# Kernel optimization log

Hardware: AMD Instinct MI355X
Metric: run time of the kernel (lower is better)

Reference implementation:

```python
import jax, jax.numpy as jnp
import numpy as np

EPS = 1e-5


def setup_inputs() -> dict:
    key = jax.random.key(0)
    ks = jax.random.split(key, 8)
    N, M, D = 8192, 8192, 512
    s = 1.0 / np.sqrt(D)
    return {
        "x": jax.random.normal(ks[0], (N, D), jnp.float32),
        "x_hat": jax.random.normal(ks[1], (1, M, D), jnp.float32),
        "Wq": jax.random.normal(ks[2], (D, D), jnp.float32) * s,
        "bq": jnp.zeros((D,), jnp.float32),
        "Wk": jax.random.normal(ks[3], (D, D), jnp.float32) * s,
        "bk": jnp.zeros((D,), jnp.float32),
        "Wv": jax.random.normal(ks[4], (D, D), jnp.float32) * s,
        "bv": jnp.zeros((D,), jnp.float32),
        "Wout": jax.random.normal(ks[5], (D, 2 * D), jnp.float32) * s,
        "bout": jnp.zeros((D,), jnp.float32),
        "gamma": jnp.ones((D,), jnp.float32),
        "beta": jnp.zeros((D,), jnp.float32),
    }


def reference(x, x_hat, Wq, bq, Wk, bk, Wv, bv, Wout, bout, gamma, beta):
    D = x.shape[-1]
    # LayerNorm over last dim
    mu = jnp.mean(x, axis=-1, keepdims=True)
    var = jnp.mean(jnp.square(x - mu), axis=-1, keepdims=True)
    xn = (x - mu) * jax.lax.rsqrt(var + EPS) * gamma + beta
    xr = xn.reshape(1, -1, D)                                   # [1, N, D]
    q = jnp.einsum('bnd,ed->bne', xr, Wq) + bq                  # [1, N, E]
    k = jnp.einsum('bmd,ed->bme', x_hat, Wk) + bk               # [1, M, E]
    qk = jnp.einsum('bne,bme->bnm', q, k) / jnp.sqrt(jnp.float32(D))
    score = jax.nn.softmax(qk, axis=-1)                         # [1, N, M]
    attn = jnp.einsum('bnm,bme->bne', score, k)                 # K used as values
    out_v = jnp.einsum('bne,fe->bnf', attn, Wv) + bv            # v-proj AFTER attention
    cat = jnp.concatenate([q, out_v], axis=-1)                  # [1, N, 2E]
    out = jnp.einsum('bnc,dc->bnd', cat, Wout) + bout           # [1, N, D]
    return out + xr
```

## Files before the change

kernel.cpp:

```cpp
#include <hip/hip_runtime.h>

typedef __attribute__((ext_vector_type(8))) short short8;
typedef __attribute__((ext_vector_type(4))) short short4v;
typedef __attribute__((ext_vector_type(4))) float f32x4;
typedef __attribute__((ext_vector_type(2))) float f32x2;

#define MFMA(a,b,c) __builtin_amdgcn_mfma_f32_16x16x32_bf16((a),(b),(c),0,0,0)

__device__ __forceinline__ short f2b(float f) {
  unsigned u = __builtin_bit_cast(unsigned, f);
  unsigned r = (u + 0x7fffu + ((u >> 16) & 1u)) >> 16;
  return (short)r;
}
__device__ __forceinline__ float b2f(short h) {
  unsigned u = ((unsigned)(unsigned short)h) << 16;
  return __builtin_bit_cast(float, u);
}
__device__ __forceinline__ unsigned pack2(float a, float b) {
  return (unsigned)(unsigned short)f2b(a) | ((unsigned)(unsigned short)f2b(b) << 16);
}

__device__ __forceinline__ float wred(float v) {
  #pragma unroll
  for (int m = 32; m; m >>= 1) v += __shfl_xor(v, m, 64);
  return v;
}

__device__ __forceinline__ void glds16(const short* g, short* l) {
  __builtin_amdgcn_global_load_lds(
      (const __attribute__((address_space(1))) unsigned*)g,
      (__attribute__((address_space(3))) unsigned*)l, 16, 0, 0);
}

__global__ __launch_bounds__(256) void cvt_kernel(const float* __restrict__ src,
                                                  short* __restrict__ dst, int n4) {
  int i = blockIdx.x * 256 + threadIdx.x;
  if (i < n4) {
    f32x4 v = *(const f32x4*)(src + (size_t)i * 4);
    short4v o = { f2b(v[0]), f2b(v[1]), f2b(v[2]), f2b(v[3]) };
    *(short4v*)(dst + (size_t)i * 4) = o;
  }
}

__global__ __launch_bounds__(256) void w2_kernel(const float* __restrict__ Wout,
                                                 const float* __restrict__ Wv,
                                                 const float* __restrict__ bvv,
                                                 const float* __restrict__ bout,
                                                 short* __restrict__ W12,
                                                 float* __restrict__ biasf) {
  int d0 = blockIdx.x * 4, tid = threadIdx.x;
  float a[4][2] = {};
  float ab[4] = {};
  for (int f = 0; f < 512; ++f) {
    f32x2 vv = *(const f32x2*)(Wv + (size_t)f * 512 + 2 * tid);
    float bvf = bvv[f];
    #pragma unroll
    for (int dd = 0; dd < 4; ++dd) {
      float wdf = Wout[(size_t)(d0 + dd) * 1024 + 512 + f];
      a[dd][0] = fmaf(wdf, vv[0], a[dd][0]);
      a[dd][1] = fmaf(wdf, vv[1], a[dd][1]);
      ab[dd] = fmaf(wdf, bvf, ab[dd]);
    }
  }
  #pragma unroll
  for (int dd = 0; dd < 4; ++dd)
    *(unsigned*)&W12[(size_t)(d0 + dd) * 1024 + 512 + 2 * tid] = pack2(a[dd][0], a[dd][1]);
  if (tid == 0) {
    #pragma unroll
    for (int dd = 0; dd < 4; ++dd) biasf[d0 + dd] = bout[d0 + dd] + ab[dd];
  }
}

__global__ __launch_bounds__(256) void ln_kernel(const float* __restrict__ x,
                                                 const float* __restrict__ gamma,
                                                 const float* __restrict__ beta,
                                                 float* __restrict__ xnf,
                                                 short* __restrict__ xnb) {
  int n = blockIdx.x, tid = threadIdx.x;
  int wid = tid >> 6, lane = tid & 63;
  f32x2 v = *(const f32x2*)(x + (size_t)n * 512 + tid * 2);
  __shared__ float red[8];
  float ws = wred(v[0] + v[1]);
  if (!lane) red[wid] = ws;
  __syncthreads();
  float mu = (red[0] + red[1] + red[2] + red[3]) * (1.f / 512.f);
  float d0 = v[0] - mu, d1 = v[1] - mu;
  ws = wred(d0 * d0 + d1 * d1);
  if (!lane) red[4 + wid] = ws;
  __syncthreads();
  float var = (red[4] + red[5] + red[6] + red[7]) * (1.f / 512.f);
  float rs = rsqrtf(var + 1e-5f);
  int c = tid * 2;
  float o0 = d0 * rs * gamma[c] + beta[c];
  float o1 = d1 * rs * gamma[c + 1] + beta[c + 1];
  *(f32x2*)(xnf + (size_t)n * 512 + c) = f32x2{ o0, o1 };
  *(unsigned*)(xnb + (size_t)n * 512 + c) = pack2(o0, o1);
}

template<int MODE>
__global__ __launch_bounds__(256, 2) void gemm_nt(
    const short* __restrict__ A, const short* __restrict__ B,
    int K, int lda, int ldb,
    const float* __restrict__ bias,
    short* __restrict__ Cb, int ldc, int coff,
    short* __restrict__ CT, int ldct,
    const float* __restrict__ resid, float* __restrict__ Cf) {
  __shared__ short As[128][72];
  __shared__ short Bs[128][72];
  int tid = threadIdx.x;
  int w = tid >> 6, lane = tid & 63;
  int li = lane & 15, g = lane >> 4;
  int wr = w >> 1, wc = w & 1;
  int bm = blockIdx.x, bn = blockIdx.y;
  f32x4 acc[4][4] = {};
  int nK = K >> 6;
  for (int kk = 0; kk < nK; ++kk) {
    short8 av[4], bv4[4];
    #pragma unroll
    for (int c = 0; c < 4; ++c) {
      int q = c * 256 + tid;
      int r = q >> 3, s = q & 7;
      av[c]  = *(const short8*)(A + (size_t)(bm * 128 + r) * lda + kk * 64 + s * 8);
      bv4[c] = *(const short8*)(B + (size_t)(bn * 128 + r) * ldb + kk * 64 + s * 8);
    }
    __syncthreads();
    #pragma unroll
    for (int c = 0; c < 4; ++c) {
      int q = c * 256 + tid;
      int r = q >> 3, s = q & 7;
      *(short8*)&As[r][s * 8] = av[c];
      *(short8*)&Bs[r][s * 8] = bv4[c];
    }
    __syncthreads();
    #pragma unroll
    for (int kc = 0; kc < 2; ++kc) {
      short8 af[4], bfr[4];
      #pragma unroll
      for (int i = 0; i < 4; ++i)
        af[i] = *(const short8*)&As[wr * 64 + i * 16 + li][kc * 32 + (g << 3)];
      #pragma unroll
      for (int j = 0; j < 4; ++j)
        bfr[j] = *(const short8*)&Bs[wc * 64 + j * 16 + li][kc * 32 + (g << 3)];
      #pragma unroll
      for (int i = 0; i < 4; ++i)
        #pragma unroll
        for (int j = 0; j < 4; ++j)
          acc[i][j] = MFMA(af[i], bfr[j], acc[i][j]);
    }
  }
  int row0 = bm * 128 + wr * 64, col0 = bn * 128 + wc * 64;
  #pragma unroll
  for (int i = 0; i < 4; ++i) {
    #pragma unroll
    for (int j = 0; j < 4; ++j) {
      int col = col0 + j * 16 + li;
      float bcol = bias[col];
      #pragma unroll
      for (int r = 0; r < 4; ++r) {
        int row = row0 + i * 16 + (g << 2) + r;
        float vv = acc[i][j][r] + bcol;
        if (MODE == 2) {
          Cf[(size_t)row * 512 + col] = vv + resid[(size_t)row * 512 + col];
        } else {
          Cb[(size_t)row * ldc + coff + col] = f2b(vv);
        }
      }
    }
  }
  if (MODE == 1) {
    #pragma unroll
    for (int i2 = 0; i2 < 2; ++i2) {
      int base = row0 + i2 * 32;
      #pragma unroll
      for (int j = 0; j < 4; ++j) {
        int col = col0 + j * 16 + li;
        float bcol = bias[col];
        #pragma unroll
        for (int r = 0; r < 4; ++r) {
          int s = (g << 2) + r;
          unsigned pk = pack2(acc[i2 * 2][j][r] + bcol, acc[i2 * 2 + 1][j][r] + bcol);
          *(unsigned*)&CT[(size_t)col * ldct + base + 2 * s] = pk;
        }
      }
    }
  }
}

#define SCALE 0.044194173824159216f
__global__ __launch_bounds__(512, 2) void attn_kernel(
    const short* __restrict__ Qg,
    const short* __restrict__ Kg,
    const short* __restrict__ KTg,
    short* __restrict__ U,
    float* __restrict__ lp) {
  __shared__ short Kl[2][32][520];
  __shared__ short Pl[2][128][32];
  int tid = threadIdx.x, w = tid >> 6, lane = tid & 63;
  int li = lane & 15, g = lane >> 4;
  int qb = blockIdx.x >> 2, ms = blockIdx.x & 3;
  int key_base = ms * 2048;

  short8 qf[16];
  {
    size_t row = (size_t)qb * 128 + w * 16 + li;
    const short* qp = Qg + row * 1024 + (g << 3);
    #pragma unroll
    for (int c = 0; c < 16; ++c) qf[c] = *(const short8*)(qp + c * 32);
  }
  f32x4 acc[8][4] = {};
  float lac[4] = {0.f, 0.f, 0.f, 0.f};

  #pragma unroll
  for (int c = 0; c < 4; ++c) {
    int r = c * 8 + w;
    glds16(Kg + (size_t)(key_base + r) * 512 + lane * 8, &Kl[0][r][0]);
  }
  __syncthreads();

  for (int t = 0; t < 64; ++t) {
    int cur = t & 1, nxt = cur ^ 1;
    if (t < 63) {
      #pragma unroll
      for (int c = 0; c < 4; ++c) {
        int r = c * 8 + w;
        glds16(Kg + (size_t)(key_base + (t + 1) * 32 + r) * 512 + lane * 8, &Kl[nxt][r][0]);
      }
    }
    short8 b2[4];
    #pragma unroll
    for (int et = 0; et < 4; ++et) {
      int e = (w << 6) + (et << 4) + li;
      b2[et] = *(const short8*)(KTg + (size_t)e * 8192 + key_base + t * 32 + (g << 3));
    }
    f32x4 s0 = {0, 0, 0, 0}, s1 = {0, 0, 0, 0};
    #pragma unroll
    for (int c = 0; c < 16; ++c) {
      short8 k0 = *(const short8*)&Kl[cur][li][c * 32 + (g << 3)];
      short8 k1 = *(const short8*)&Kl[cur][16 + li][c * 32 + (g << 3)];
      s0 = MFMA(qf[c], k0, s0);
      s1 = MFMA(qf[c], k1, s1);
    }
    #pragma unroll
    for (int r = 0; r < 4; ++r) {
      float p0 = __expf(s0[r] * SCALE);
      float p1 = __expf(s1[r] * SCALE);
      lac[r] += p0 + p1;
      int prow = (w << 4) + (g << 2) + r;
      *(unsigned*)&Pl[cur][prow][2 * li] = pack2(p0, p1);
    }
    __syncthreads();
    #pragma unroll
    for (int qt = 0; qt < 8; ++qt) {
      short8 a = *(const short8*)&Pl[cur][qt * 16 + li][g << 3];
      #pragma unroll
      for (int et = 0; et < 4; ++et)
        acc[qt][et] = MFMA(a, b2[et], acc[qt][et]);
    }
  }

  short* Up = U + (((size_t)ms * 8192) + (size_t)qb * 128) * 512;
  #pragma unroll
  for (int qt = 0; qt < 8; ++qt)
    #pragma unroll
    for (int et = 0; et < 4; ++et)
      #pragma unroll
      for (int r = 0; r < 4; ++r) {
        int row = (qt << 4) + (g << 2) + r;
        int col = (w << 6) + (et << 4) + li;
        Up[(size_t)row * 512 + col] = f2b(acc[qt][et][r]);
      }
  #pragma unroll
  for (int r = 0; r < 4; ++r) {
    float v = lac[r];
    v += __shfl_xor(v, 1, 16);
    v += __shfl_xor(v, 2, 16);
    v += __shfl_xor(v, 4, 16);
    v += __shfl_xor(v, 8, 16);
    if (!li) lp[ms * 8192 + qb * 128 + (w << 4) + (g << 2) + r] = v;
  }
}

__global__ __launch_bounds__(256) void combine_kernel(const short* __restrict__ U,
                                                      const float* __restrict__ lp,
                                                      short* __restrict__ cat2) {
  int idx = blockIdx.x * 256 + threadIdx.x;
  int n = idx >> 6, e8 = (idx & 63) << 3;
  float s[8] = {0, 0, 0, 0, 0, 0, 0, 0};
  float li = 0.f;
  #pragma unroll
  for (int msv = 0; msv < 4; ++msv) {
    short8 v = *(const short8*)(U + ((size_t)msv * 8192 + n) * 512 + e8);
    #pragma unroll
    for (int j = 0; j < 8; ++j) s[j] += b2f(v[j]);
    li += lp[msv * 8192 + n];
  }
  float inv = 1.f / li;
  short8 o;
  #pragma unroll
  for (int j = 0; j < 8; ++j) o[j] = f2b(s[j] * inv);
  *(short8*)(cat2 + (size_t)n * 1024 + 512 + e8) = o;
}

extern "C" void kernel_launch(void* const* d_in, const int* in_sizes, int n_in,
                              void* d_out, int out_size, void* d_ws, size_t ws_size,
                              hipStream_t stream) {
  const float* x     = (const float*)d_in[0];
  const float* xhat  = (const float*)d_in[1];
  const float* Wq    = (const float*)d_in[2];
  const float* bq    = (const float*)d_in[3];
  const float* Wk    = (const float*)d_in[4];
  const float* bk    = (const float*)d_in[5];
  const float* Wv    = (const float*)d_in[6];
  const float* bv    = (const float*)d_in[7];
  const float* Wout  = (const float*)d_in[8];
  const float* bout  = (const float*)d_in[9];
  const float* gamma = (const float*)d_in[10];
  const float* beta  = (const float*)d_in[11];
  float* out = (float*)d_out;

  char* ws = (char*)d_ws;
  const size_t MB = 1024 * 1024;
  float* xnf  = (float*)(ws + 0);
  short* cat2 = (short*)(ws + 16 * MB);
  short* kb   = (short*)(ws + 32 * MB);
  short* ktb  = (short*)(ws + 40 * MB);
  short* W12  = (short*)(ws + 48 * MB);
  float* bsf  = (float*)(ws + 49 * MB);
  float* lp   = (float*)(ws + 49 * MB + 65536);
  short* U    = (short*)(ws + 52 * MB);
  short* xnb  = (short*)(ws + 52 * MB);
  short* xhb  = (short*)(ws + 60 * MB);
  short* Wqb  = (short*)(ws + 68 * MB);
  short* Wkb  = (short*)(ws + 69 * MB);
  (void)ws_size; (void)in_sizes; (void)n_in; (void)out_size;

  cvt_kernel<<<4096, 256, 0, stream>>>(xhat, xhb, 1048576);
  cvt_kernel<<<256, 256, 0, stream>>>(Wq, Wqb, 65536);
  cvt_kernel<<<256, 256, 0, stream>>>(Wk, Wkb, 65536);
  cvt_kernel<<<512, 256, 0, stream>>>(Wout, W12, 131072);
  w2_kernel<<<128, 256, 0, stream>>>(Wout, Wv, bv, bout, W12, bsf);
  ln_kernel<<<8192, 256, 0, stream>>>(x, gamma, beta, xnf, xnb);
  gemm_nt<0><<<dim3(64, 4), 256, 0, stream>>>(xnb, Wqb, 512, 512, 512, bq,
                                              cat2, 1024, 0, nullptr, 0, nullptr, nullptr);
  gemm_nt<1><<<dim3(64, 4), 256, 0, stream>>>(xhb, Wkb, 512, 512, 512, bk,
                                              kb, 512, 0, ktb, 8192, nullptr, nullptr);
  attn_kernel<<<256, 512, 0, stream>>>(cat2, kb, ktb, U, lp);
  combine_kernel<<<2048, 256, 0, stream>>>(U, lp, cat2);
  gemm_nt<2><<<dim3(64, 4), 256, 0, stream>>>(cat2, W12, 1024, 1024, 1024, bsf,
                                              nullptr, 0, 0, nullptr, 0, xnf, out);
}
```

Baseline: 347.9 us.

## Replace scalar Wout·Wv fold with MFMA GEMM, vectorize LayerNorm, add setprio

The scalar w2_kernel that folded Wv into Wout is replaced by three steps: a transposed bf16 conversion of Wv, a small bias-reduction kernel, and the existing MFMA gemm_nt run on bf16 copies. LayerNorm now handles one row per wavefront with 8-wide vector loads and no shared-memory barriers. The K-transpose store in the K-projection GEMM writes 8-byte packed stores, and the attention kernel raises wave priority around its MFMA loops. The weight product is now computed from bf16 inputs instead of fp32, which slightly changes numerics, and the change adds several extra kernel launches.

```diff
diff --git a/kernel.cpp b/kernel.cpp
--- a/kernel.cpp
+++ b/kernel.cpp
@@ -4,6 +4,7 @@
 typedef __attribute__((ext_vector_type(4))) short short4v;
 typedef __attribute__((ext_vector_type(4))) float f32x4;
 typedef __attribute__((ext_vector_type(2))) float f32x2;
+typedef __attribute__((ext_vector_type(2))) unsigned uint2v;
 
 #define MFMA(a,b,c) __builtin_amdgcn_mfma_f32_16x16x32_bf16((a),(b),(c),0,0,0)
 
@@ -42,33 +43,35 @@
   }
 }
 
-__global__ __launch_bounds__(256) void w2_kernel(const float* __restrict__ Wout,
-                                                 const float* __restrict__ Wv,
-                                                 const float* __restrict__ bvv,
-                                                 const float* __restrict__ bout,
-                                                 short* __restrict__ W12,
-                                                 float* __restrict__ biasf) {
-  int d0 = blockIdx.x * 4, tid = threadIdx.x;
-  float a[4][2] = {};
-  float ab[4] = {};
-  for (int f = 0; f < 512; ++f) {
-    f32x2 vv = *(const f32x2*)(Wv + (size_t)f * 512 + 2 * tid);
-    float bvf = bvv[f];
-    #pragma unroll
-    for (int dd = 0; dd < 4; ++dd) {
-      float wdf = Wout[(size_t)(d0 + dd) * 1024 + 512 + f];
-      a[dd][0] = fmaf(wdf, vv[0], a[dd][0]);
-      a[dd][1] = fmaf(wdf, vv[1], a[dd][1]);
-      ab[dd] = fmaf(wdf, bvf, ab[dd]);
-    }
-  }
-  #pragma unroll
-  for (int dd = 0; dd < 4; ++dd)
-    *(unsigned*)&W12[(size_t)(d0 + dd) * 1024 + 512 + 2 * tid] = pack2(a[dd][0], a[dd][1]);
-  if (tid == 0) {
-    #pragma unroll
-    for (int dd = 0; dd < 4; ++dd) biasf[d0 + dd] = bout[d0 + dd] + ab[dd];
-  }
+__global__ __launch_bounds__(256) void tcvt_kernel(const float* __restrict__ src,
+                                                   short* __restrict__ dst) {
+  __shared__ float tile[32][33];
+  int bx = blockIdx.x & 15, by = blockIdx.x >> 4;
+  int tx = threadIdx.x & 31, ty = threadIdx.x >> 5;
+  #pragma unroll
+  for (int i = 0; i < 4; ++i)
+    tile[ty + 8 * i][tx] = src[(size_t)(by * 32 + ty + 8 * i) * 512 + bx * 32 + tx];
+  __syncthreads();
+  #pragma unroll
+  for (int i = 0; i < 4; ++i)
+    dst[(size_t)(bx * 32 + ty + 8 * i) * 512 + by * 32 + tx] = f2b(tile[tx][ty + 8 * i]);
+}
+
+__global__ __launch_bounds__(256) void bsf_kernel(const float* __restrict__ Wout,
+                                                  const float* __restrict__ bvv,
+                                                  const float* __restrict__ bout,
+                                                  float* __restrict__ biasf,
+                                                  float* __restrict__ zb) {
+  int d = blockIdx.x, tid = threadIdx.x;
+  int wid = tid >> 6, lane = tid & 63;
+  __shared__ float red[4];
+  float s = Wout[(size_t)d * 1024 + 512 + tid] * bvv[tid]
+          + Wout[(size_t)d * 1024 + 768 + tid] * bvv[tid + 256];
+  s = wred(s);
+  if (!lane) red[wid] = s;
+  __syncthreads();
+  if (!tid) biasf[d] = bout[d] + red[0] + red[1] + red[2] + red[3];
+  if (d == 0) { zb[tid] = 0.f; zb[tid + 256] = 0.f; }
 }
 
 __global__ __launch_bounds__(256) void ln_kernel(const float* __restrict__ x,
@@ -76,25 +79,29 @@
                                                  const float* __restrict__ beta,
                                                  float* __restrict__ xnf,
                                                  short* __restrict__ xnb) {
-  int n = blockIdx.x, tid = threadIdx.x;
-  int wid = tid >> 6, lane = tid & 63;
-  f32x2 v = *(const f32x2*)(x + (size_t)n * 512 + tid * 2);
-  __shared__ float red[8];
-  float ws = wred(v[0] + v[1]);
-  if (!lane) red[wid] = ws;
-  __syncthreads();
-  float mu = (red[0] + red[1] + red[2] + red[3]) * (1.f / 512.f);
-  float d0 = v[0] - mu, d1 = v[1] - mu;
-  ws = wred(d0 * d0 + d1 * d1);
-  if (!lane) red[4 + wid] = ws;
-  __syncthreads();
-  float var = (red[4] + red[5] + red[6] + red[7]) * (1.f / 512.f);
+  int wid = threadIdx.x >> 6, lane = threadIdx.x & 63;
+  int n = blockIdx.x * 4 + wid;
+  const float* xp = x + (size_t)n * 512 + lane * 8;
+  f32x4 v0 = *(const f32x4*)xp;
+  f32x4 v1 = *(const f32x4*)(xp + 4);
+  float s = v0[0] + v0[1] + v0[2] + v0[3] + v1[0] + v1[1] + v1[2] + v1[3];
+  float mu = wred(s) * (1.f / 512.f);
+  f32x4 d0 = v0 - mu, d1 = v1 - mu;
+  float q = d0[0]*d0[0] + d0[1]*d0[1] + d0[2]*d0[2] + d0[3]*d0[3]
+          + d1[0]*d1[0] + d1[1]*d1[1] + d1[2]*d1[2] + d1[3]*d1[3];
+  float var = wred(q) * (1.f / 512.f);
   float rs = rsqrtf(var + 1e-5f);
-  int c = tid * 2;
-  float o0 = d0 * rs * gamma[c] + beta[c];
-  float o1 = d1 * rs * gamma[c + 1] + beta[c + 1];
-  *(f32x2*)(xnf + (size_t)n * 512 + c) = f32x2{ o0, o1 };
-  *(unsigned*)(xnb + (size_t)n * 512 + c) = pack2(o0, o1);
+  int c = lane * 8;
+  f32x4 g0 = *(const f32x4*)(gamma + c), g1 = *(const f32x4*)(gamma + c + 4);
+  f32x4 b0 = *(const f32x4*)(beta + c),  b1 = *(const f32x4*)(beta + c + 4);
+  f32x4 o0 = d0 * rs * g0 + b0;
+  f32x4 o1 = d1 * rs * g1 + b1;
+  float* op = xnf + (size_t)n * 512 + c;
+  *(f32x4*)op = o0;
+  *(f32x4*)(op + 4) = o1;
+  short8 ob = { f2b(o0[0]), f2b(o0[1]), f2b(o0[2]), f2b(o0[3]),
+                f2b(o1[0]), f2b(o1[1]), f2b(o1[2]), f2b(o1[3]) };
+  *(short8*)(xnb + (size_t)n * 512 + c) = ob;
 }
 
 template<int MODE>
@@ -176,10 +183,12 @@
         int col = col0 + j * 16 + li;
         float bcol = bias[col];
         #pragma unroll
-        for (int r = 0; r < 4; ++r) {
-          int s = (g << 2) + r;
-          unsigned pk = pack2(acc[i2 * 2][j][r] + bcol, acc[i2 * 2 + 1][j][r] + bcol);
-          *(unsigned*)&CT[(size_t)col * ldct + base + 2 * s] = pk;
+        for (int rp = 0; rp < 2; ++rp) {
+          int r = rp * 2;
+          uint2v pk;
+          pk[0] = pack2(acc[i2 * 2][j][r]     + bcol, acc[i2 * 2 + 1][j][r]     + bcol);
+          pk[1] = pack2(acc[i2 * 2][j][r + 1] + bcol, acc[i2 * 2 + 1][j][r + 1] + bcol);
+          *(uint2v*)&CT[(size_t)col * ldct + base + 8 * g + 2 * r] = pk;
         }
       }
     }
@@ -233,6 +242,7 @@
       b2[et] = *(const short8*)(KTg + (size_t)e * 8192 + key_base + t * 32 + (g << 3));
     }
     f32x4 s0 = {0, 0, 0, 0}, s1 = {0, 0, 0, 0};
+    __builtin_amdgcn_s_setprio(1);
     #pragma unroll
     for (int c = 0; c < 16; ++c) {
       short8 k0 = *(const short8*)&Kl[cur][li][c * 32 + (g << 3)];
@@ -240,6 +250,7 @@
       s0 = MFMA(qf[c], k0, s0);
       s1 = MFMA(qf[c], k1, s1);
     }
+    __builtin_amdgcn_s_setprio(0);
     #pragma unroll
     for (int r = 0; r < 4; ++r) {
       float p0 = __expf(s0[r] * SCALE);
@@ -249,6 +260,7 @@
       *(unsigned*)&Pl[cur][prow][2 * li] = pack2(p0, p1);
     }
     __syncthreads();
+    __builtin_amdgcn_s_setprio(1);
     #pragma unroll
     for (int qt = 0; qt < 8; ++qt) {
       short8 a = *(const short8*)&Pl[cur][qt * 16 + li][g << 3];
@@ -256,6 +268,7 @@
       for (int et = 0; et < 4; ++et)
         acc[qt][et] = MFMA(a, b2[et], acc[qt][et]);
     }
+    __builtin_amdgcn_s_setprio(0);
   }
 
   short* Up = U + (((size_t)ms * 8192) + (size_t)qb * 128) * 512;
@@ -320,26 +333,33 @@
 
   char* ws = (char*)d_ws;
   const size_t MB = 1024 * 1024;
-  float* xnf  = (float*)(ws + 0);
-  short* cat2 = (short*)(ws + 16 * MB);
-  short* kb   = (short*)(ws + 32 * MB);
-  short* ktb  = (short*)(ws + 40 * MB);
-  short* W12  = (short*)(ws + 48 * MB);
-  float* bsf  = (float*)(ws + 49 * MB);
-  float* lp   = (float*)(ws + 49 * MB + 65536);
-  short* U    = (short*)(ws + 52 * MB);
-  short* xnb  = (short*)(ws + 52 * MB);
-  short* xhb  = (short*)(ws + 60 * MB);
-  short* Wqb  = (short*)(ws + 68 * MB);
-  short* Wkb  = (short*)(ws + 69 * MB);
+  float* xnf   = (float*)(ws + 0);
+  short* cat2  = (short*)(ws + 16 * MB);
+  short* kb    = (short*)(ws + 32 * MB);
+  short* ktb   = (short*)(ws + 40 * MB);
+  short* W12   = (short*)(ws + 48 * MB);
+  float* bsf   = (float*)(ws + 49 * MB);
+  float* lp    = (float*)(ws + 49 * MB + 65536);
+  short* Woutb = (short*)(ws + 50 * MB);
+  short* WvTb  = (short*)(ws + 51 * MB);
+  float* zb    = (float*)(ws + 51 * MB + 524288);
+  short* U     = (short*)(ws + 52 * MB);
+  short* xnb   = (short*)(ws + 52 * MB);
+  short* xhb   = (short*)(ws + 60 * MB);
+  short* Wqb   = (short*)(ws + 68 * MB);
+  short* Wkb   = (short*)(ws + 69 * MB);
   (void)ws_size; (void)in_sizes; (void)n_in; (void)out_size;
 
   cvt_kernel<<<4096, 256, 0, stream>>>(xhat, xhb, 1048576);
   cvt_kernel<<<256, 256, 0, stream>>>(Wq, Wqb, 65536);
   cvt_kernel<<<256, 256, 0, stream>>>(Wk, Wkb, 65536);
   cvt_kernel<<<512, 256, 0, stream>>>(Wout, W12, 131072);
-  w2_kernel<<<128, 256, 0, stream>>>(Wout, Wv, bv, bout, W12, bsf);
-  ln_kernel<<<8192, 256, 0, stream>>>(x, gamma, beta, xnf, xnb);
+  cvt_kernel<<<512, 256, 0, stream>>>(Wout, Woutb, 131072);
+  tcvt_kernel<<<256, 256, 0, stream>>>(Wv, WvTb);
+  bsf_kernel<<<512, 256, 0, stream>>>(Wout, bv, bout, bsf, zb);
+  gemm_nt<0><<<dim3(4, 4), 256, 0, stream>>>(Woutb + 512, WvTb, 512, 1024, 512, zb,
+                                             W12, 1024, 512, nullptr, 0, nullptr, nullptr);
+  ln_kernel<<<2048, 256, 0, stream>>>(x, gamma, beta, xnf, xnb);
   gemm_nt<0><<<dim3(64, 4), 256, 0, stream>>>(xnb, Wqb, 512, 512, 512, bq,
                                               cat2, 1024, 0, nullptr, 0, nullptr, nullptr);
   gemm_nt<1><<<dim3(64, 4), 256, 0, stream>>>(xhb, Wkb, 512, 512, 512, bk,
```

Measured after the change: 374.1 us. +7.5%, slower.
